# Kernel optimization log

Hardware: AMD Instinct MI355X
Metric: run time of the kernel (lower is better)

The kernel has to match this reference:

```python
import jax, jax.numpy as jnp
import numpy as np

B, N, C, K = 8, 4096, 128, 16
POOL_RATE = 4  # npoint = N // POOL_RATE


def setup_inputs() -> dict:
    key = jax.random.key(0)
    k1, k2, k3 = jax.random.split(key, 3)
    vertices = jax.random.normal(k1, (B, 3, N), dtype=jnp.float32)
    feature_map = jax.random.normal(k2, (B, C, N), dtype=jnp.float32)
    # pre-flattened global knn indices, values in [0, B*N) as produced upstream
    idx = jax.random.randint(k3, (B * N * K,), 0, B * N, dtype=jnp.int64)
    return {"vertices": vertices, "feature_map": feature_map, "idx": idx}


def farthest_point_sample(xyz, npoint):
    """xyz: (B, N, 3) -> centroid indices (B, npoint).
    Deterministic start at index 0 (torch version uses a random start)."""
    b, n, _ = xyz.shape

    def step(carry, _):
        distance, farthest = carry
        centroid = jnp.take_along_axis(xyz, farthest[:, None, None], axis=1)  # (B,1,3)
        dist = jnp.sum((xyz - centroid) ** 2, axis=-1)  # (B,N)
        distance = jnp.minimum(distance, dist)
        new_farthest = jnp.argmax(distance, axis=-1)
        return (distance, new_farthest), farthest

    dist0 = jnp.full((b, n), 1e10, dtype=xyz.dtype)
    far0 = jnp.zeros((b,), dtype=jnp.int32)
    _, cents = jax.lax.scan(step, (dist0, far0), None, length=npoint)
    return cents.T  # (B, npoint)


def reference(vertices, feature_map, idx):
    b, c, n = feature_map.shape
    # get_graph_feature with precomputed flat idx: gather neighbors then max-pool
    flat = feature_map.transpose(0, 2, 1).reshape(b * n, c)        # (B*N, C)
    neigh = flat[idx].reshape(b, n, K, c)                          # (B,N,K,C)
    pooled = jnp.max(neigh, axis=2)                                # (B,N,C) == (B,C,N) pooled_feature, channel-last

    npoint = n // POOL_RATE
    xyz = vertices.transpose(0, 2, 1)                              # (B,N,3)
    cents = farthest_point_sample(xyz, npoint)                     # (B,npoint)

    vertices_pool = jnp.take_along_axis(xyz, cents[:, :, None], axis=1).transpose(0, 2, 1)     # (B,3,npoint)
    feature_map_pool = jnp.take_along_axis(pooled, cents[:, :, None], axis=1).transpose(0, 2, 1)  # (B,C,npoint)
    return (vertices_pool, feature_map_pool)
```

## Files before the change

### kernel.cpp

```cpp
#include <hip/hip_runtime.h>
#include <hip/hip_bf16.h>
#include <math.h>

#define B_SZ 8
#define N_SZ 4096
#define C_SZ 128
#define K_SZ 16
#define NPOINT 1024

#define FPS_T 256
#define FPS_PAIRS 8

typedef float vf2 __attribute__((ext_vector_type(2)));

template <int CTRL>
__device__ __forceinline__ double dpp_dmax_step(double k) {
    const unsigned long long u = __builtin_bit_cast(unsigned long long, k);
    const int lo = (int)(unsigned)u;
    const int hi = (int)(unsigned)(u >> 32);
    const unsigned lo2 = (unsigned)__builtin_amdgcn_update_dpp(0, lo, CTRL, 0xF, 0xF, true);
    const unsigned hi2 = (unsigned)__builtin_amdgcn_update_dpp(0, hi, CTRL, 0xF, 0xF, true);
    const double k2 = __builtin_bit_cast(double,
        ((unsigned long long)hi2 << 32) | (unsigned long long)lo2);
    return fmax(k, k2);
}
__device__ __forceinline__ double wave_dmax63(double k) {
    k = dpp_dmax_step<0x111>(k);
    k = dpp_dmax_step<0x112>(k);
    k = dpp_dmax_step<0x114>(k);
    k = dpp_dmax_step<0x118>(k);
    k = dpp_dmax_step<0x142>(k);
    k = dpp_dmax_step<0x143>(k);
    return k;
}

__global__ void transpose_fm(const float* __restrict__ fm, float* __restrict__ fmT) {
    __shared__ float tile[32][33];
    const int b  = blockIdx.z;
    const int c0 = blockIdx.y * 32;
    const int n0 = blockIdx.x * 32;
    const int tx = threadIdx.x;
    const int ty = threadIdx.y;
    const float* p = fm + (size_t)b * C_SZ * N_SZ;
#pragma unroll
    for (int i = 0; i < 4; i++) {
        tile[ty + i * 8][tx] = p[(size_t)(c0 + ty + i * 8) * N_SZ + n0 + tx];
    }
    __syncthreads();
    float* q = fmT + (size_t)b * N_SZ * C_SZ;
#pragma unroll
    for (int i = 0; i < 4; i++) {
        q[(size_t)(n0 + ty + i * 8) * C_SZ + c0 + tx] = tile[tx][ty + i * 8];
    }
}

__global__ __launch_bounds__(FPS_T) void fps_kernel(
        const float* __restrict__ verts,
        float* __restrict__ out_vp,
        int* __restrict__ cents)
{
#pragma clang fp contract(off)
#pragma clang fp reassociate(off)
    __shared__ float4 sp[N_SZ];
    __shared__ int    scent[NPOINT];
    __shared__ alignas(16) double ckey[2][4];

    const int b    = blockIdx.x;
    const int tid  = threadIdx.x;
    const int lane = tid & 63;
    const int wid  = tid >> 6;
    const float* vb = verts + (size_t)b * 3 * N_SZ;

    vf2 px[FPS_PAIRS], py[FPS_PAIRS], pz[FPS_PAIRS], dd[FPS_PAIRS];
#pragma unroll
    for (int p = 0; p < FPS_PAIRS; p++) {
        const int n0 = tid + (2 * p) * FPS_T;
        const int n1 = n0 + FPS_T;
        const float x0 = vb[n0],            x1 = vb[n1];
        const float y0 = vb[N_SZ + n0],     y1 = vb[N_SZ + n1];
        const float z0 = vb[2 * N_SZ + n0], z1 = vb[2 * N_SZ + n1];
        px[p] = (vf2){x0, x1};
        py[p] = (vf2){y0, y1};
        pz[p] = (vf2){z0, z1};
        dd[p] = (vf2){1e10f, 1e10f};
        sp[n0] = make_float4(x0, y0, z0, 0.0f);
        sp[n1] = make_float4(x1, y1, z1, 0.0f);
    }
    __syncthreads();

    int ci = 0;
    float4 c0 = sp[0];
    float cx = c0.x, cy = c0.y, cz = c0.z;

    for (int i = 0; i < NPOINT; i++) {
        if (tid == 0) scent[i] = ci;

        const vf2 cx2 = (vf2){cx, cx};
        const vf2 cy2 = (vf2){cy, cy};
        const vf2 cz2 = (vf2){cz, cz};

        float m0 = -1.0f, m1 = -1.0f;
#pragma unroll
        for (int p = 0; p < FPS_PAIRS; p++) {
            const vf2 dx = px[p] - cx2;
            const vf2 dy = py[p] - cy2;
            const vf2 dz = pz[p] - cz2;
            vf2 s = dx * dx + dy * dy;
            s = s + dz * dz;
            vf2 d;
            d.x = fminf(dd[p].x, s.x);
            d.y = fminf(dd[p].y, s.y);
            dd[p] = d;
            m0 = fmaxf(m0, d.x);
            m1 = fmaxf(m1, d.y);
        }
        const float bv = fmaxf(m0, m1);

        int bj = 0;
#pragma unroll
        for (int j = 15; j >= 0; j--) {
            const float v = (j & 1) ? dd[j >> 1].y : dd[j >> 1].x;
            if (v == bv) bj = j;
        }

        const unsigned n = (unsigned)(tid + (bj << 8));
        double key = __builtin_bit_cast(double,
            ((unsigned long long)__float_as_uint(bv) << 32) |
            (unsigned long long)(4095u - n));

        key = wave_dmax63(key);
        const int par = i & 1;
        if (lane == 63) ckey[par][wid] = key;
        __syncthreads();

        const double2* kb = (const double2*)(&ckey[par][0]);
        const double2 k01 = kb[0], k23 = kb[1];
        const double kk = fmax(fmax(k01.x, k01.y), fmax(k23.x, k23.y));

        ci = (int)(4095u - (unsigned)__builtin_bit_cast(unsigned long long, kk));
        const float4 c = sp[ci];
        cx = c.x; cy = c.y; cz = c.z;
    }
    __syncthreads();

    for (int i = tid; i < NPOINT; i += FPS_T) {
        const int cc = scent[i];
        const float4 v = sp[cc];
        cents[b * NPOINT + i] = cc;
        out_vp[(b * 3 + 0) * NPOINT + i] = v.x;
        out_vp[(b * 3 + 1) * NPOINT + i] = v.y;
        out_vp[(b * 3 + 2) * NPOINT + i] = v.z;
    }
}

#define GT_J 16
__global__ __launch_bounds__(1024) void pool_gather_t(
        const float* __restrict__ fmT,
        const int* __restrict__ idx,
        const int* __restrict__ cents,
        float* __restrict__ out_fp)
{
    __shared__ float tile[C_SZ][GT_J + 1];
    const int tid  = threadIdx.x;
    const int lane = tid & 63;
    const int w    = tid >> 6;
    const int j0   = blockIdx.x * GT_J;
    const int gp   = j0 + w;
    const int b    = gp >> 10;
    const int ci   = cents[gp];
    const int* ip  = idx + ((size_t)(b * N_SZ + ci)) * K_SZ;
    const float2* src = (const float2*)fmT;

    float2 acc = make_float2(-INFINITY, -INFINITY);
#pragma unroll
    for (int k = 0; k < K_SZ; k++) {
        const int p = ip[k];
        const float2 v = src[(size_t)p * (C_SZ / 2) + lane];
        acc.x = fmaxf(acc.x, v.x);
        acc.y = fmaxf(acc.y, v.y);
    }
    tile[2 * lane][w]     = acc.x;
    tile[2 * lane + 1][w] = acc.y;
    __syncthreads();

    float* q = out_fp + (size_t)b * C_SZ * NPOINT + (j0 & (NPOINT - 1));
#pragma unroll
    for (int it = 0; it < 2; it++) {
        const int e  = tid + it * 1024;
        const int c  = e >> 4;
        const int jj = e & (GT_J - 1);
        q[(size_t)c * NPOINT + jj] = tile[c][jj];
    }
}

extern "C" void kernel_launch(void* const* d_in, const int* in_sizes, int n_in,
                              void* d_out, int out_size, void* d_ws, size_t ws_size,
                              hipStream_t stream) {
    const float* verts = (const float*)d_in[0];
    const float* fm    = (const float*)d_in[1];
    const int*   idx   = (const int*)d_in[2];

    float* out    = (float*)d_out;
    float* out_vp = out;
    float* out_fp = out + (size_t)B_SZ * 3 * NPOINT;

    char* ws = (char*)d_ws;
    float* fmT   = (float*)ws;
    int*   cents = (int*)(ws + (size_t)B_SZ * N_SZ * C_SZ * 4);

    dim3 tb(32, 8);
    transpose_fm<<<dim3(N_SZ / 32, C_SZ / 32, B_SZ), tb, 0, stream>>>(fm, fmT);
    fps_kernel<<<B_SZ, FPS_T, 0, stream>>>(verts, out_vp, cents);
    pool_gather_t<<<(B_SZ * NPOINT) / GT_J, 1024, 0, stream>>>(fmT, idx, cents, out_fp);
}
```

Measured before the change: 643.5 us.

## Replace double-key DPP argmax with float wave max plus ballot index select

The per-iteration argmax in farthest point sampling now runs a float-only DPP max reduction, then a readlane, a ballot and a find-first-set to pick the lowest-index lane holding the max, instead of a 64-bit packed double-key reduction that needed two DPP moves per step. Point ownership changes to contiguous blocks of 16 per thread, loaded with float4 vector loads, so the ballot's first lane corresponds to the smallest global index. Cross-wave combining uses 64-bit integer keys. This shortens the serial critical path of each of the 1024 FPS iterations, at the cost of extra scalar/readlane instructions.

```diff
diff --git a/kernel.cpp b/kernel.cpp
--- a/kernel.cpp
+++ b/kernel.cpp
@@ -14,24 +14,22 @@
 typedef float vf2 __attribute__((ext_vector_type(2)));
 
 template <int CTRL>
-__device__ __forceinline__ double dpp_dmax_step(double k) {
-    const unsigned long long u = __builtin_bit_cast(unsigned long long, k);
-    const int lo = (int)(unsigned)u;
-    const int hi = (int)(unsigned)(u >> 32);
-    const unsigned lo2 = (unsigned)__builtin_amdgcn_update_dpp(0, lo, CTRL, 0xF, 0xF, true);
-    const unsigned hi2 = (unsigned)__builtin_amdgcn_update_dpp(0, hi, CTRL, 0xF, 0xF, true);
-    const double k2 = __builtin_bit_cast(double,
-        ((unsigned long long)hi2 << 32) | (unsigned long long)lo2);
-    return fmax(k, k2);
-}
-__device__ __forceinline__ double wave_dmax63(double k) {
-    k = dpp_dmax_step<0x111>(k);
-    k = dpp_dmax_step<0x112>(k);
-    k = dpp_dmax_step<0x114>(k);
-    k = dpp_dmax_step<0x118>(k);
-    k = dpp_dmax_step<0x142>(k);
-    k = dpp_dmax_step<0x143>(k);
-    return k;
+__device__ __forceinline__ float dpp_fmax(float x) {
+    int t = __builtin_amdgcn_update_dpp(0, __float_as_int(x), CTRL, 0xF, 0xF, true);
+    return fmaxf(x, __int_as_float(t));
+}
+__device__ __forceinline__ float wave_fmax63(float x) {
+    x = dpp_fmax<0x111>(x);
+    x = dpp_fmax<0x112>(x);
+    x = dpp_fmax<0x114>(x);
+    x = dpp_fmax<0x118>(x);
+    x = dpp_fmax<0x142>(x);
+    x = dpp_fmax<0x143>(x);
+    return x;
+}
+__device__ __forceinline__ unsigned long long kmax2(unsigned long long a,
+                                                   unsigned long long b) {
+    return a > b ? a : b;
 }
 
 __global__ void transpose_fm(const float* __restrict__ fm, float* __restrict__ fmT) {
@@ -63,7 +61,7 @@
 #pragma clang fp reassociate(off)
     __shared__ float4 sp[N_SZ];
     __shared__ int    scent[NPOINT];
-    __shared__ alignas(16) double ckey[2][4];
+    __shared__ alignas(16) unsigned long long ckey[2][4];
 
     const int b    = blockIdx.x;
     const int tid  = threadIdx.x;
@@ -71,25 +69,29 @@
     const int wid  = tid >> 6;
     const float* vb = verts + (size_t)b * 3 * N_SZ;
 
+    for (int n = tid; n < N_SZ; n += FPS_T) {
+        sp[n] = make_float4(vb[n], vb[N_SZ + n], vb[2 * N_SZ + n], 0.0f);
+    }
+
+    const float4* vx4 = (const float4*)vb;
+    const float4* vy4 = (const float4*)(vb + N_SZ);
+    const float4* vz4 = (const float4*)(vb + 2 * N_SZ);
     vf2 px[FPS_PAIRS], py[FPS_PAIRS], pz[FPS_PAIRS], dd[FPS_PAIRS];
 #pragma unroll
-    for (int p = 0; p < FPS_PAIRS; p++) {
-        const int n0 = tid + (2 * p) * FPS_T;
-        const int n1 = n0 + FPS_T;
-        const float x0 = vb[n0],            x1 = vb[n1];
-        const float y0 = vb[N_SZ + n0],     y1 = vb[N_SZ + n1];
-        const float z0 = vb[2 * N_SZ + n0], z1 = vb[2 * N_SZ + n1];
-        px[p] = (vf2){x0, x1};
-        py[p] = (vf2){y0, y1};
-        pz[p] = (vf2){z0, z1};
-        dd[p] = (vf2){1e10f, 1e10f};
-        sp[n0] = make_float4(x0, y0, z0, 0.0f);
-        sp[n1] = make_float4(x1, y1, z1, 0.0f);
+    for (int k = 0; k < 4; k++) {
+        const float4 x = vx4[tid * 4 + k];
+        const float4 y = vy4[tid * 4 + k];
+        const float4 z = vz4[tid * 4 + k];
+        px[2 * k] = (vf2){x.x, x.y}; px[2 * k + 1] = (vf2){x.z, x.w};
+        py[2 * k] = (vf2){y.x, y.y}; py[2 * k + 1] = (vf2){y.z, y.w};
+        pz[2 * k] = (vf2){z.x, z.y}; pz[2 * k + 1] = (vf2){z.z, z.w};
+        dd[2 * k]     = (vf2){1e10f, 1e10f};
+        dd[2 * k + 1] = (vf2){1e10f, 1e10f};
     }
     __syncthreads();
 
     int ci = 0;
-    float4 c0 = sp[0];
+    const float4 c0 = sp[0];
     float cx = c0.x, cy = c0.y, cz = c0.z;
 
     for (int i = 0; i < NPOINT; i++) {
@@ -99,7 +101,7 @@
         const vf2 cy2 = (vf2){cy, cy};
         const vf2 cz2 = (vf2){cz, cz};
 
-        float m0 = -1.0f, m1 = -1.0f;
+        float m = -1.0f;
 #pragma unroll
         for (int p = 0; p < FPS_PAIRS; p++) {
             const vf2 dx = px[p] - cx2;
@@ -111,10 +113,9 @@
             d.x = fminf(dd[p].x, s.x);
             d.y = fminf(dd[p].y, s.y);
             dd[p] = d;
-            m0 = fmaxf(m0, d.x);
-            m1 = fmaxf(m1, d.y);
+            m = fmaxf(m, fmaxf(d.x, d.y));
         }
-        const float bv = fmaxf(m0, m1);
+        const float bv = m;
 
         int bj = 0;
 #pragma unroll
@@ -122,22 +123,29 @@
             const float v = (j & 1) ? dd[j >> 1].y : dd[j >> 1].x;
             if (v == bv) bj = j;
         }
-
-        const unsigned n = (unsigned)(tid + (bj << 8));
-        double key = __builtin_bit_cast(double,
-            ((unsigned long long)__float_as_uint(bv) << 32) |
-            (unsigned long long)(4095u - n));
-
-        key = wave_dmax63(key);
+        const int bn = (tid << 4) | bj;
+
+        const float wm = wave_fmax63(bv);
+        const float wmax = __int_as_float(
+            __builtin_amdgcn_readlane(__float_as_int(wm), 63));
+        const unsigned long long mask = __ballot(bv == wmax);
+        const int first = __ffsll(mask) - 1;
+        const unsigned nw = (unsigned)__builtin_amdgcn_readlane(bn, first);
+
+        const unsigned long long wkey =
+            ((unsigned long long)__float_as_uint(wmax) << 32) |
+            (unsigned long long)(4095u - nw);
+
         const int par = i & 1;
-        if (lane == 63) ckey[par][wid] = key;
+        if (lane == 0) ckey[par][wid] = wkey;
         __syncthreads();
 
-        const double2* kb = (const double2*)(&ckey[par][0]);
-        const double2 k01 = kb[0], k23 = kb[1];
-        const double kk = fmax(fmax(k01.x, k01.y), fmax(k23.x, k23.y));
-
-        ci = (int)(4095u - (unsigned)__builtin_bit_cast(unsigned long long, kk));
+        const ulonglong2* kb = (const ulonglong2*)(&ckey[par][0]);
+        const ulonglong2 k01 = kb[0], k23 = kb[1];
+        const unsigned long long kk =
+            kmax2(kmax2(k01.x, k01.y), kmax2(k23.x, k23.y));
+
+        ci = (int)(4095u - (unsigned)kk);
         const float4 c = sp[ci];
         cx = c.x; cy = c.y; cz = c.z;
     }
```

Result: faster. 612.1 us (-4.9%).
